# Optimization experiments

Hardware: AMD Instinct MI355X
Metric: run time of the kernel (lower is better)

The kernel has to match this reference:

```python
import jax, jax.numpy as jnp
import numpy as np

BRANCH = [True, False] * 10  # branchLs: joints that also emit a tracking frame
TRACK_IDX = np.where(np.array(BRANCH))[0]


def rpy2r(rpy):
    # rpy (..., 3) -> rotation (..., 3, 3), R = Rz(yaw) @ Ry(pitch) @ Rx(roll)
    r, p, y = rpy[..., 0], rpy[..., 1], rpy[..., 2]
    cr, sr = jnp.cos(r), jnp.sin(r)
    cp, sp = jnp.cos(p), jnp.sin(p)
    cy, sy = jnp.cos(y), jnp.sin(y)
    return jnp.stack([
        jnp.stack([cy * cp, cy * sp * sr - sy * cr, cy * sp * cr + sy * sr], -1),
        jnp.stack([sy * cp, sy * sp * sr + cy * cr, sy * sp * cr - cy * sr], -1),
        jnp.stack([-sp, cp * sr, cp * cr], -1)], -2)


def pr2t(p, R):
    # p (...,3), R (...,3,3) -> homogeneous transform (...,4,4)
    top = jnp.concatenate([R, p[..., None]], axis=-1)
    bot = jnp.broadcast_to(jnp.array([0., 0., 0., 1.], R.dtype), top.shape[:-2] + (1, 4))
    return jnp.concatenate([top, bot], axis=-2)


def rodrigues(axis, q):
    # axis (J,3) (normalized inside), q (B,J) angles -> (B,J,3,3)
    a = axis / (jnp.linalg.norm(axis, axis=-1, keepdims=True) + 1e-12)
    ax, ay, az = a[..., 0], a[..., 1], a[..., 2]
    z = jnp.zeros_like(ax)
    K = jnp.stack([jnp.stack([z, -az, ay], -1),
                   jnp.stack([az, z, -ax], -1),
                   jnp.stack([-ay, ax, z], -1)], -2)  # (J,3,3)
    K2 = K @ K
    s = jnp.sin(q)[..., None, None]  # (B,J,1,1)
    c = jnp.cos(q)[..., None, None]
    return jnp.eye(3, dtype=q.dtype) + s * K + (1. - c) * K2


def _forward(rev_q, pri_q, rev_p_off, rev_rpy_off, pri_p_off, pri_rpy_off,
             rev_axis, pri_axis, p_track, rpy_track):
    B, J = rev_q.shape
    dt = rev_q.dtype
    rev_T_off = pr2t(rev_p_off, rpy2r(rev_rpy_off))    # (J,4,4)
    pri_T_off = pr2t(pri_p_off, rpy2r(pri_rpy_off))    # (J,4,4)
    T_track = pr2t(p_track, rpy2r(rpy_track))          # (J,4,4)
    rev_T = pr2t(jnp.zeros((B, J, 3), dt), rodrigues(rev_axis, rev_q))  # (B,J,4,4)
    eye3 = jnp.broadcast_to(jnp.eye(3, dtype=dt), (B, J, 3, 3))
    pri_T = pr2t(pri_q[..., None] * pri_axis[None], eye3)               # (B,J,4,4)
    # fold constant offsets into per-joint steps, joint axis leading for scan
    rev_step = jnp.einsum('jab,njbc->jnac', rev_T_off, rev_T)  # (J,B,4,4)
    pri_step = jnp.einsum('jab,njbc->jnac', pri_T_off, pri_T)  # (J,B,4,4)

    def step(out, xs):
        rs, ps, tt = xs
        out1 = out @ rs          # after revolute joint
        out2 = out1 @ ps         # after prismatic joint
        return out2, (out1, out2, out2 @ tt)

    init = jnp.broadcast_to(jnp.eye(4, dtype=dt), (B, 4, 4))
    _, (rev_all, pri_all, trk_all) = jax.lax.scan(step, init, (rev_step, pri_step, T_track))
    RevSE3 = jnp.transpose(rev_all, (1, 0, 2, 3))                  # (B,J,4,4)
    PriSE3 = jnp.transpose(pri_all, (1, 0, 2, 3))                  # (B,J,4,4)
    TrackingSE3 = jnp.transpose(trk_all[TRACK_IDX], (1, 0, 2, 3))  # (B,n_track,4,4)
    return TrackingSE3, RevSE3, PriSE3


def setup_inputs() -> dict:
    key = jax.random.key(0)
    ks = jax.random.split(key, 10)
    B, J = 32768, 20
    u = lambda k, s: jax.random.uniform(k, s, jnp.float32, -1., 1.)
    return {
        'rev_q_value': jax.random.normal(ks[0], (B, J), jnp.float32),
        'pri_q_value': jax.random.normal(ks[1], (B, J), jnp.float32),
        'rev_p_offset': u(ks[2], (J, 3)), 'rev_rpy_offset': u(ks[3], (J, 3)),
        'pri_p_offset': u(ks[4], (J, 3)), 'pri_rpy_offset': u(ks[5], (J, 3)),
        'rev_axis': u(ks[6], (J, 3)), 'pri_axis': u(ks[7], (J, 3)),
        'p_track': u(ks[8], (J, 3)), 'rpy_track': u(ks[9], (J, 3)),
    }


def reference(rev_q_value, pri_q_value, rev_p_offset, rev_rpy_offset,
              pri_p_offset, pri_rpy_offset, rev_axis, pri_axis, p_track, rpy_track):
    return _forward(rev_q_value, pri_q_value, rev_p_offset, rev_rpy_offset,
                    pri_p_offset, pri_rpy_offset, rev_axis, pri_axis, p_track, rpy_track)
```

## Files before the change

kernel.cpp:

```cpp
#include <hip/hip_runtime.h>
#include <math.h>


constexpr int NJ = 20;

__device__ __forceinline__ void rpy2r_dev(float r, float p, float y, float R[9]) {
    float sr, cr, sp, cp, sy, cy;
    __sincosf(r, &sr, &cr);
    __sincosf(p, &sp, &cp);
    __sincosf(y, &sy, &cy);
    R[0] = cy * cp; R[1] = cy * sp * sr - sy * cr; R[2] = cy * sp * cr + sy * sr;
    R[3] = sy * cp; R[4] = sy * sp * sr + cy * cr; R[5] = sy * sp * cr - cy * sr;
    R[6] = -sp;     R[7] = cp * sr;                R[8] = cp * cr;
}

__device__ __forceinline__ void mat33_mul(const float A[9], const float B[9], float C[9]) {
#pragma unroll
    for (int i = 0; i < 3; ++i) {
        C[3 * i + 0] = A[3 * i + 0] * B[0] + A[3 * i + 1] * B[3] + A[3 * i + 2] * B[6];
        C[3 * i + 1] = A[3 * i + 0] * B[1] + A[3 * i + 1] * B[4] + A[3 * i + 2] * B[7];
        C[3 * i + 2] = A[3 * i + 0] * B[2] + A[3 * i + 1] * B[5] + A[3 * i + 2] * B[8];
    }
}

__global__ __launch_bounds__(64) void fk_kernel(
    const float* __restrict__ rev_q,      const float* __restrict__ pri_q,
    const float* __restrict__ rev_p_off,  const float* __restrict__ rev_rpy_off,
    const float* __restrict__ pri_p_off,  const float* __restrict__ pri_rpy_off,
    const float* __restrict__ rev_axis,   const float* __restrict__ pri_axis,
    const float* __restrict__ p_track,    const float* __restrict__ rpy_track,
    float* __restrict__ out, int B)
{
    __shared__ float4 cst[NJ][11];
    const int t = threadIdx.x;

    if (t < NJ) {
        const int j = t;
        float Ro[9], Rp[9], Rt[9];
        rpy2r_dev(rev_rpy_off[3 * j], rev_rpy_off[3 * j + 1], rev_rpy_off[3 * j + 2], Ro);
        rpy2r_dev(pri_rpy_off[3 * j], pri_rpy_off[3 * j + 1], pri_rpy_off[3 * j + 2], Rp);
        rpy2r_dev(rpy_track[3 * j],   rpy_track[3 * j + 1],   rpy_track[3 * j + 2],   Rt);
        cst[j][0] = make_float4(Ro[0], Ro[1], Ro[2], rev_p_off[3 * j + 0]);
        cst[j][1] = make_float4(Ro[3], Ro[4], Ro[5], rev_p_off[3 * j + 1]);
        cst[j][2] = make_float4(Ro[6], Ro[7], Ro[8], rev_p_off[3 * j + 2]);
        cst[j][3] = make_float4(Rp[0], Rp[1], Rp[2], pri_p_off[3 * j + 0]);
        cst[j][4] = make_float4(Rp[3], Rp[4], Rp[5], pri_p_off[3 * j + 1]);
        cst[j][5] = make_float4(Rp[6], Rp[7], Rp[8], pri_p_off[3 * j + 2]);
        cst[j][6] = make_float4(Rt[0], Rt[1], Rt[2], p_track[3 * j + 0]);
        cst[j][7] = make_float4(Rt[3], Rt[4], Rt[5], p_track[3 * j + 1]);
        cst[j][8] = make_float4(Rt[6], Rt[7], Rt[8], p_track[3 * j + 2]);
        const float ax = rev_axis[3 * j], ay = rev_axis[3 * j + 1], az = rev_axis[3 * j + 2];
        const float inv = 1.0f / (sqrtf(ax * ax + ay * ay + az * az) + 1e-12f);
        cst[j][9] = make_float4(ax * inv, ay * inv, az * inv, 0.0f);
        const float px = pri_axis[3 * j], py = pri_axis[3 * j + 1], pz = pri_axis[3 * j + 2];
        cst[j][10] = make_float4(Rp[0] * px + Rp[1] * py + Rp[2] * pz,
                                 Rp[3] * px + Rp[4] * py + Rp[5] * pz,
                                 Rp[6] * px + Rp[7] * py + Rp[8] * pz, 0.0f);
    }
    __syncthreads();

    const int b = blockIdx.x * 64 + t;
    if (b >= B) return;

    float rq[NJ], pq[NJ];
    {
        const float4* r4 = reinterpret_cast<const float4*>(rev_q + (size_t)b * NJ);
        const float4* p4 = reinterpret_cast<const float4*>(pri_q + (size_t)b * NJ);
#pragma unroll
        for (int i = 0; i < NJ / 4; ++i) {
            float4 a = r4[i];
            rq[4 * i + 0] = a.x; rq[4 * i + 1] = a.y; rq[4 * i + 2] = a.z; rq[4 * i + 3] = a.w;
            float4 c = p4[i];
            pq[4 * i + 0] = c.x; pq[4 * i + 1] = c.y; pq[4 * i + 2] = c.z; pq[4 * i + 3] = c.w;
        }
    }

    float TR[9] = {1, 0, 0, 0, 1, 0, 0, 0, 1};
    float Tp[3] = {0, 0, 0};

    float4* out4 = reinterpret_cast<float4*>(out);
    const size_t trkBase = (size_t)b * 40;
    const size_t revBase = (size_t)B * 40 + (size_t)b * 80;
    const size_t priBase = (size_t)B * 120 + (size_t)b * 80;

#pragma unroll
    for (int j = 0; j < NJ; ++j) {
        float s, c;
        __sincosf(rq[j], &s, &c);
        const float4 a4 = cst[j][9];
        const float ax = a4.x, ay = a4.y, az = a4.z;
        const float omc = 1.0f - c;
        float Rr[9];
        Rr[0] = c + omc * ax * ax;      Rr[1] = omc * ax * ay - s * az; Rr[2] = omc * ax * az + s * ay;
        Rr[3] = omc * ax * ay + s * az; Rr[4] = c + omc * ay * ay;      Rr[5] = omc * ay * az - s * ax;
        Rr[6] = omc * ax * az - s * ay; Rr[7] = omc * ay * az + s * ax; Rr[8] = c + omc * az * az;

        const float4 cr0 = cst[j][0], cr1 = cst[j][1], cr2 = cst[j][2];
        const float Roff[9] = {cr0.x, cr0.y, cr0.z, cr1.x, cr1.y, cr1.z, cr2.x, cr2.y, cr2.z};
        float Ra[9], R1[9], p1[3];
        mat33_mul(TR, Roff, Ra);
        mat33_mul(Ra, Rr, R1);
#pragma unroll
        for (int i = 0; i < 3; ++i)
            p1[i] = fmaf(TR[3 * i + 0], cr0.w,
                    fmaf(TR[3 * i + 1], cr1.w,
                    fmaf(TR[3 * i + 2], cr2.w, Tp[i])));

        out4[revBase + 4 * j + 0] = make_float4(R1[0], R1[1], R1[2], p1[0]);
        out4[revBase + 4 * j + 1] = make_float4(R1[3], R1[4], R1[5], p1[1]);
        out4[revBase + 4 * j + 2] = make_float4(R1[6], R1[7], R1[8], p1[2]);
        out4[revBase + 4 * j + 3] = make_float4(0.f, 0.f, 0.f, 1.f);

        const float4 cp0 = cst[j][3], cp1 = cst[j][4], cp2 = cst[j][5];
        const float4 w4 = cst[j][10];
        const float qp = pq[j];
        const float pstep[3] = {fmaf(qp, w4.x, cp0.w), fmaf(qp, w4.y, cp1.w), fmaf(qp, w4.z, cp2.w)};
        const float Rpoff[9] = {cp0.x, cp0.y, cp0.z, cp1.x, cp1.y, cp1.z, cp2.x, cp2.y, cp2.z};
        float R2[9], p2[3];
        mat33_mul(R1, Rpoff, R2);
#pragma unroll
        for (int i = 0; i < 3; ++i)
            p2[i] = fmaf(R1[3 * i + 0], pstep[0],
                    fmaf(R1[3 * i + 1], pstep[1],
                    fmaf(R1[3 * i + 2], pstep[2], p1[i])));

        out4[priBase + 4 * j + 0] = make_float4(R2[0], R2[1], R2[2], p2[0]);
        out4[priBase + 4 * j + 1] = make_float4(R2[3], R2[4], R2[5], p2[1]);
        out4[priBase + 4 * j + 2] = make_float4(R2[6], R2[7], R2[8], p2[2]);
        out4[priBase + 4 * j + 3] = make_float4(0.f, 0.f, 0.f, 1.f);

        if ((j & 1) == 0) {
            const float4 ct0 = cst[j][6], ct1 = cst[j][7], ct2 = cst[j][8];
            const float Rtrk[9] = {ct0.x, ct0.y, ct0.z, ct1.x, ct1.y, ct1.z, ct2.x, ct2.y, ct2.z};
            float R3[9], p3[3];
            mat33_mul(R2, Rtrk, R3);
#pragma unroll
            for (int i = 0; i < 3; ++i)
                p3[i] = fmaf(R2[3 * i + 0], ct0.w,
                        fmaf(R2[3 * i + 1], ct1.w,
                        fmaf(R2[3 * i + 2], ct2.w, p2[i])));
            const size_t tb = trkBase + 4 * (size_t)(j >> 1);
            out4[tb + 0] = make_float4(R3[0], R3[1], R3[2], p3[0]);
            out4[tb + 1] = make_float4(R3[3], R3[4], R3[5], p3[1]);
            out4[tb + 2] = make_float4(R3[6], R3[7], R3[8], p3[2]);
            out4[tb + 3] = make_float4(0.f, 0.f, 0.f, 1.f);
        }

#pragma unroll
        for (int i = 0; i < 9; ++i) TR[i] = R2[i];
#pragma unroll
        for (int i = 0; i < 3; ++i) Tp[i] = p2[i];
    }
}

extern "C" void kernel_launch(void* const* d_in, const int* in_sizes, int n_in,
                              void* d_out, int out_size, void* d_ws, size_t ws_size,
                              hipStream_t stream) {
    (void)n_in; (void)out_size; (void)d_ws; (void)ws_size;
    const float* rev_q       = (const float*)d_in[0];
    const float* pri_q       = (const float*)d_in[1];
    const float* rev_p_off   = (const float*)d_in[2];
    const float* rev_rpy_off = (const float*)d_in[3];
    const float* pri_p_off   = (const float*)d_in[4];
    const float* pri_rpy_off = (const float*)d_in[5];
    const float* rev_axis    = (const float*)d_in[6];
    const float* pri_axis    = (const float*)d_in[7];
    const float* p_track     = (const float*)d_in[8];
    const float* rpy_track   = (const float*)d_in[9];

    const int B = in_sizes[0] / NJ;
    const int blocks = (B + 63) / 64;
    fk_kernel<<<dim3(blocks), dim3(64), 0, stream>>>(
        rev_q, pri_q, rev_p_off, rev_rpy_off, pri_p_off, pri_rpy_off,
        rev_axis, pri_axis, p_track, rpy_track, (float*)d_out, B);
}
```

Measured before the change: 169.3 us.

## Split FK into prefix-transform pass and parallel per-joint output pass

The kernel now runs in two phases. First, 64 threads compute the serial chain of prefix transforms per batch element and store them in LDS. Then all 256 threads process the (batch, joint) pairs independently, recomputing each joint's rev/pri/track transforms from the stored prefix and writing outputs. This exposes more parallelism for the store-heavy output phase and makes writes across threads more interleaved. The cost is duplicated per-joint math, about 60KB of shared memory per block (which limits occupancy), and 3/4 of the threads sitting idle during the serial phase.

```diff
diff --git a/kernel.cpp b/kernel.cpp
--- a/kernel.cpp
+++ b/kernel.cpp
@@ -3,6 +3,8 @@
 
 
 constexpr int NJ = 20;
+constexpr int GB = 64;
+constexpr int PREF_STRIDE = 61;
 
 __device__ __forceinline__ void rpy2r_dev(float r, float p, float y, float R[9]) {
     float sr, cr, sp, cp, sy, cy;
@@ -23,7 +25,7 @@
     }
 }
 
-__global__ __launch_bounds__(64) void fk_kernel(
+__global__ __launch_bounds__(256) void fk_kernel(
     const float* __restrict__ rev_q,      const float* __restrict__ pri_q,
     const float* __restrict__ rev_p_off,  const float* __restrict__ rev_rpy_off,
     const float* __restrict__ pri_p_off,  const float* __restrict__ pri_rpy_off,
@@ -32,6 +34,10 @@
     float* __restrict__ out, int B)
 {
     __shared__ float4 cst[NJ][11];
+    __shared__ float4 pre4[GB * PREF_STRIDE];
+    __shared__ float  sRq[GB * NJ];
+    __shared__ float  sPq[GB * NJ];
+
     const int t = threadIdx.x;
 
     if (t < NJ) {
@@ -59,37 +65,87 @@
     }
     __syncthreads();
 
-    const int b = blockIdx.x * 64 + t;
-    if (b >= B) return;
-
-    float rq[NJ], pq[NJ];
-    {
-        const float4* r4 = reinterpret_cast<const float4*>(rev_q + (size_t)b * NJ);
-        const float4* p4 = reinterpret_cast<const float4*>(pri_q + (size_t)b * NJ);
-#pragma unroll
-        for (int i = 0; i < NJ / 4; ++i) {
-            float4 a = r4[i];
-            rq[4 * i + 0] = a.x; rq[4 * i + 1] = a.y; rq[4 * i + 2] = a.z; rq[4 * i + 3] = a.w;
-            float4 c = p4[i];
-            pq[4 * i + 0] = c.x; pq[4 * i + 1] = c.y; pq[4 * i + 2] = c.z; pq[4 * i + 3] = c.w;
+    const int blockBase = blockIdx.x * GB;
+
+    if (t < GB) {
+        const int b = blockBase + t;
+        if (b < B) {
+            float rq[NJ], pq[NJ];
+            const float4* r4 = reinterpret_cast<const float4*>(rev_q + (size_t)b * NJ);
+            const float4* p4 = reinterpret_cast<const float4*>(pri_q + (size_t)b * NJ);
+            float4* sR4 = reinterpret_cast<float4*>(&sRq[t * NJ]);
+            float4* sP4 = reinterpret_cast<float4*>(&sPq[t * NJ]);
+#pragma unroll
+            for (int i = 0; i < NJ / 4; ++i) {
+                float4 a = r4[i]; sR4[i] = a;
+                rq[4 * i] = a.x; rq[4 * i + 1] = a.y; rq[4 * i + 2] = a.z; rq[4 * i + 3] = a.w;
+                float4 c = p4[i]; sP4[i] = c;
+                pq[4 * i] = c.x; pq[4 * i + 1] = c.y; pq[4 * i + 2] = c.z; pq[4 * i + 3] = c.w;
+            }
+
+            float TR[9] = {1, 0, 0, 0, 1, 0, 0, 0, 1};
+            float Tp[3] = {0, 0, 0};
+#pragma unroll
+            for (int j = 0; j < NJ; ++j) {
+                float4* pr = &pre4[t * PREF_STRIDE + j * 3];
+                pr[0] = make_float4(TR[0], TR[1], TR[2], Tp[0]);
+                pr[1] = make_float4(TR[3], TR[4], TR[5], Tp[1]);
+                pr[2] = make_float4(TR[6], TR[7], TR[8], Tp[2]);
+
+                float s, c;
+                __sincosf(rq[j], &s, &c);
+                const float4 a4 = cst[j][9];
+                const float ax = a4.x, ay = a4.y, az = a4.z, omc = 1.0f - c;
+                float Rr[9];
+                Rr[0] = c + omc * ax * ax;      Rr[1] = omc * ax * ay - s * az; Rr[2] = omc * ax * az + s * ay;
+                Rr[3] = omc * ax * ay + s * az; Rr[4] = c + omc * ay * ay;      Rr[5] = omc * ay * az - s * ax;
+                Rr[6] = omc * ax * az - s * ay; Rr[7] = omc * ay * az + s * ax; Rr[8] = c + omc * az * az;
+
+                const float4 cr0 = cst[j][0], cr1 = cst[j][1], cr2 = cst[j][2];
+                const float Roff[9] = {cr0.x, cr0.y, cr0.z, cr1.x, cr1.y, cr1.z, cr2.x, cr2.y, cr2.z};
+                float Ra[9], R1[9], p1[3];
+                mat33_mul(TR, Roff, Ra);
+                mat33_mul(Ra, Rr, R1);
+#pragma unroll
+                for (int i = 0; i < 3; ++i)
+                    p1[i] = fmaf(TR[3 * i], cr0.w, fmaf(TR[3 * i + 1], cr1.w, fmaf(TR[3 * i + 2], cr2.w, Tp[i])));
+
+                const float4 cp0 = cst[j][3], cp1 = cst[j][4], cp2 = cst[j][5];
+                const float4 w4 = cst[j][10];
+                const float qp = pq[j];
+                const float pstep[3] = {fmaf(qp, w4.x, cp0.w), fmaf(qp, w4.y, cp1.w), fmaf(qp, w4.z, cp2.w)};
+                const float Rpoff[9] = {cp0.x, cp0.y, cp0.z, cp1.x, cp1.y, cp1.z, cp2.x, cp2.y, cp2.z};
+                float R2[9];
+                mat33_mul(R1, Rpoff, R2);
+#pragma unroll
+                for (int i = 0; i < 3; ++i)
+                    Tp[i] = fmaf(R1[3 * i], pstep[0], fmaf(R1[3 * i + 1], pstep[1], fmaf(R1[3 * i + 2], pstep[2], p1[i])));
+#pragma unroll
+                for (int i = 0; i < 9; ++i) TR[i] = R2[i];
+            }
         }
     }
-
-    float TR[9] = {1, 0, 0, 0, 1, 0, 0, 0, 1};
-    float Tp[3] = {0, 0, 0};
+    __syncthreads();
 
     float4* out4 = reinterpret_cast<float4*>(out);
-    const size_t trkBase = (size_t)b * 40;
-    const size_t revBase = (size_t)B * 40 + (size_t)b * 80;
-    const size_t priBase = (size_t)B * 120 + (size_t)b * 80;
-
-#pragma unroll
-    for (int j = 0; j < NJ; ++j) {
+    const int npairs = GB * NJ;
+#pragma unroll
+    for (int it = 0; it < npairs / 256; ++it) {
+        const int p = it * 256 + t;
+        const int bl = (p * 3277) >> 16;
+        const int j = p - bl * 20;
+        const int b = blockBase + bl;
+        if (b >= B) continue;
+
+        const float4* pr = &pre4[bl * PREF_STRIDE + j * 3];
+        const float4 t0 = pr[0], t1 = pr[1], t2 = pr[2];
+        const float TbR[9] = {t0.x, t0.y, t0.z, t1.x, t1.y, t1.z, t2.x, t2.y, t2.z};
+        const float Tbp[3] = {t0.w, t1.w, t2.w};
+
         float s, c;
-        __sincosf(rq[j], &s, &c);
+        __sincosf(sRq[bl * NJ + j], &s, &c);
         const float4 a4 = cst[j][9];
-        const float ax = a4.x, ay = a4.y, az = a4.z;
-        const float omc = 1.0f - c;
+        const float ax = a4.x, ay = a4.y, az = a4.z, omc = 1.0f - c;
         float Rr[9];
         Rr[0] = c + omc * ax * ax;      Rr[1] = omc * ax * ay - s * az; Rr[2] = omc * ax * az + s * ay;
         Rr[3] = omc * ax * ay + s * az; Rr[4] = c + omc * ay * ay;      Rr[5] = omc * ay * az - s * ax;
@@ -98,36 +154,34 @@
         const float4 cr0 = cst[j][0], cr1 = cst[j][1], cr2 = cst[j][2];
         const float Roff[9] = {cr0.x, cr0.y, cr0.z, cr1.x, cr1.y, cr1.z, cr2.x, cr2.y, cr2.z};
         float Ra[9], R1[9], p1[3];
-        mat33_mul(TR, Roff, Ra);
+        mat33_mul(TbR, Roff, Ra);
         mat33_mul(Ra, Rr, R1);
 #pragma unroll
         for (int i = 0; i < 3; ++i)
-            p1[i] = fmaf(TR[3 * i + 0], cr0.w,
-                    fmaf(TR[3 * i + 1], cr1.w,
-                    fmaf(TR[3 * i + 2], cr2.w, Tp[i])));
-
-        out4[revBase + 4 * j + 0] = make_float4(R1[0], R1[1], R1[2], p1[0]);
-        out4[revBase + 4 * j + 1] = make_float4(R1[3], R1[4], R1[5], p1[1]);
-        out4[revBase + 4 * j + 2] = make_float4(R1[6], R1[7], R1[8], p1[2]);
-        out4[revBase + 4 * j + 3] = make_float4(0.f, 0.f, 0.f, 1.f);
+            p1[i] = fmaf(TbR[3 * i], cr0.w, fmaf(TbR[3 * i + 1], cr1.w, fmaf(TbR[3 * i + 2], cr2.w, Tbp[i])));
+
+        const size_t revBase = (size_t)B * 40 + (size_t)b * 80 + (size_t)j * 4;
+        out4[revBase + 0] = make_float4(R1[0], R1[1], R1[2], p1[0]);
+        out4[revBase + 1] = make_float4(R1[3], R1[4], R1[5], p1[1]);
+        out4[revBase + 2] = make_float4(R1[6], R1[7], R1[8], p1[2]);
+        out4[revBase + 3] = make_float4(0.f, 0.f, 0.f, 1.f);
 
         const float4 cp0 = cst[j][3], cp1 = cst[j][4], cp2 = cst[j][5];
         const float4 w4 = cst[j][10];
-        const float qp = pq[j];
+        const float qp = sPq[bl * NJ + j];
         const float pstep[3] = {fmaf(qp, w4.x, cp0.w), fmaf(qp, w4.y, cp1.w), fmaf(qp, w4.z, cp2.w)};
         const float Rpoff[9] = {cp0.x, cp0.y, cp0.z, cp1.x, cp1.y, cp1.z, cp2.x, cp2.y, cp2.z};
         float R2[9], p2[3];
         mat33_mul(R1, Rpoff, R2);
 #pragma unroll
         for (int i = 0; i < 3; ++i)
-            p2[i] = fmaf(R1[3 * i + 0], pstep[0],
-                    fmaf(R1[3 * i + 1], pstep[1],
-                    fmaf(R1[3 * i + 2], pstep[2], p1[i])));
-
-        out4[priBase + 4 * j + 0] = make_float4(R2[0], R2[1], R2[2], p2[0]);
-        out4[priBase + 4 * j + 1] = make_float4(R2[3], R2[4], R2[5], p2[1]);
-        out4[priBase + 4 * j + 2] = make_float4(R2[6], R2[7], R2[8], p2[2]);
-        out4[priBase + 4 * j + 3] = make_float4(0.f, 0.f, 0.f, 1.f);
+            p2[i] = fmaf(R1[3 * i], pstep[0], fmaf(R1[3 * i + 1], pstep[1], fmaf(R1[3 * i + 2], pstep[2], p1[i])));
+
+        const size_t priBase = (size_t)B * 120 + (size_t)b * 80 + (size_t)j * 4;
+        out4[priBase + 0] = make_float4(R2[0], R2[1], R2[2], p2[0]);
+        out4[priBase + 1] = make_float4(R2[3], R2[4], R2[5], p2[1]);
+        out4[priBase + 2] = make_float4(R2[6], R2[7], R2[8], p2[2]);
+        out4[priBase + 3] = make_float4(0.f, 0.f, 0.f, 1.f);
 
         if ((j & 1) == 0) {
             const float4 ct0 = cst[j][6], ct1 = cst[j][7], ct2 = cst[j][8];
@@ -136,20 +190,13 @@
             mat33_mul(R2, Rtrk, R3);
 #pragma unroll
             for (int i = 0; i < 3; ++i)
-                p3[i] = fmaf(R2[3 * i + 0], ct0.w,
-                        fmaf(R2[3 * i + 1], ct1.w,
-                        fmaf(R2[3 * i + 2], ct2.w, p2[i])));
-            const size_t tb = trkBase + 4 * (size_t)(j >> 1);
+                p3[i] = fmaf(R2[3 * i], ct0.w, fmaf(R2[3 * i + 1], ct1.w, fmaf(R2[3 * i + 2], ct2.w, p2[i])));
+            const size_t tb = (size_t)b * 40 + (size_t)(j >> 1) * 4;
             out4[tb + 0] = make_float4(R3[0], R3[1], R3[2], p3[0]);
             out4[tb + 1] = make_float4(R3[3], R3[4], R3[5], p3[1]);
             out4[tb + 2] = make_float4(R3[6], R3[7], R3[8], p3[2]);
             out4[tb + 3] = make_float4(0.f, 0.f, 0.f, 1.f);
         }
-
-#pragma unroll
-        for (int i = 0; i < 9; ++i) TR[i] = R2[i];
-#pragma unroll
-        for (int i = 0; i < 3; ++i) Tp[i] = p2[i];
     }
 }
 
@@ -169,8 +216,8 @@
     const float* rpy_track   = (const float*)d_in[9];
 
     const int B = in_sizes[0] / NJ;
-    const int blocks = (B + 63) / 64;
-    fk_kernel<<<dim3(blocks), dim3(64), 0, stream>>>(
+    const int blocks = (B + GB - 1) / GB;
+    fk_kernel<<<dim3(blocks), dim3(256), 0, stream>>>(
         rev_q, pri_q, rev_p_off, rev_rpy_off, pri_p_off, pri_rpy_off,
         rev_axis, pri_axis, p_track, rpy_track, (float*)d_out, B);
 }
```

Result: faster. 152.0 us (-10.2%).

## Parallelize joint chain with wave-level prefix scan over affine transforms

Applied to the files above, without the earlier changes.

Replaces the per-thread sequential 20-joint forward-kinematics loop with one lane per (batch, joint). Each lane builds its local step transform, and an inclusive prefix scan over 3x4 affine compositions runs via __shfl_up across 32-lane segments. This spreads the serial dependency chain across lanes and makes adjacent lanes write adjacent joint matrices, which coalesces stores. In exchange it does more total arithmetic (log-step composes and many shuffles) and leaves 12 of every 32 lanes idle.

```diff
diff --git a/kernel.cpp b/kernel.cpp
--- a/kernel.cpp
+++ b/kernel.cpp
@@ -3,6 +3,9 @@
 
 
 constexpr int NJ = 20;
+constexpr int BPB = 8;
+
+struct Aff { float R[9]; float p[3]; };
 
 __device__ __forceinline__ void rpy2r_dev(float r, float p, float y, float R[9]) {
     float sr, cr, sp, cp, sy, cy;
@@ -23,7 +26,27 @@
     }
 }
 
-__global__ __launch_bounds__(64) void fk_kernel(
+__device__ __forceinline__ Aff compose(const Aff& A, const Aff& B) {
+    Aff C;
+    mat33_mul(A.R, B.R, C.R);
+#pragma unroll
+    for (int i = 0; i < 3; ++i)
+        C.p[i] = fmaf(A.R[3 * i + 0], B.p[0],
+                 fmaf(A.R[3 * i + 1], B.p[1],
+                 fmaf(A.R[3 * i + 2], B.p[2], A.p[i])));
+    return C;
+}
+
+__device__ __forceinline__ Aff shfl_up_aff(const Aff& V, int d) {
+    Aff N;
+#pragma unroll
+    for (int k = 0; k < 9; ++k) N.R[k] = __shfl_up(V.R[k], d, 32);
+#pragma unroll
+    for (int k = 0; k < 3; ++k) N.p[k] = __shfl_up(V.p[k], d, 32);
+    return N;
+}
+
+__global__ __launch_bounds__(256) void fk_scan_kernel(
     const float* __restrict__ rev_q,      const float* __restrict__ pri_q,
     const float* __restrict__ rev_p_off,  const float* __restrict__ rev_rpy_off,
     const float* __restrict__ pri_p_off,  const float* __restrict__ pri_rpy_off,
@@ -59,97 +82,84 @@
     }
     __syncthreads();
 
-    const int b = blockIdx.x * 64 + t;
-    if (b >= B) return;
+    const int j = t & 31;
+    const int b = blockIdx.x * BPB + (t >> 5);
+    if (j >= NJ || b >= B) return;
 
-    float rq[NJ], pq[NJ];
-    {
-        const float4* r4 = reinterpret_cast<const float4*>(rev_q + (size_t)b * NJ);
-        const float4* p4 = reinterpret_cast<const float4*>(pri_q + (size_t)b * NJ);
+    const float rq = rev_q[(size_t)b * NJ + j];
+    const float pq = pri_q[(size_t)b * NJ + j];
+
+    float s, c;
+    __sincosf(rq, &s, &c);
+    const float4 a4 = cst[j][9];
+    const float ax = a4.x, ay = a4.y, az = a4.z, omc = 1.0f - c;
+    float Rr[9];
+    Rr[0] = c + omc * ax * ax;      Rr[1] = omc * ax * ay - s * az; Rr[2] = omc * ax * az + s * ay;
+    Rr[3] = omc * ax * ay + s * az; Rr[4] = c + omc * ay * ay;      Rr[5] = omc * ay * az - s * ax;
+    Rr[6] = omc * ax * az - s * ay; Rr[7] = omc * ay * az + s * ax; Rr[8] = c + omc * az * az;
+
+    const float4 cr0 = cst[j][0], cr1 = cst[j][1], cr2 = cst[j][2];
+    const float Roff[9] = {cr0.x, cr0.y, cr0.z, cr1.x, cr1.y, cr1.z, cr2.x, cr2.y, cr2.z};
+    Aff revstep;
+    mat33_mul(Roff, Rr, revstep.R);
+    revstep.p[0] = cr0.w; revstep.p[1] = cr1.w; revstep.p[2] = cr2.w;
+
+    const float4 cp0 = cst[j][3], cp1 = cst[j][4], cp2 = cst[j][5];
+    const float4 w4 = cst[j][10];
+    const float Rpoff[9] = {cp0.x, cp0.y, cp0.z, cp1.x, cp1.y, cp1.z, cp2.x, cp2.y, cp2.z};
+    const float pp[3] = {fmaf(pq, w4.x, cp0.w), fmaf(pq, w4.y, cp1.w), fmaf(pq, w4.z, cp2.w)};
+
+    Aff V;
+    mat33_mul(revstep.R, Rpoff, V.R);
 #pragma unroll
-        for (int i = 0; i < NJ / 4; ++i) {
-            float4 a = r4[i];
-            rq[4 * i + 0] = a.x; rq[4 * i + 1] = a.y; rq[4 * i + 2] = a.z; rq[4 * i + 3] = a.w;
-            float4 c = p4[i];
-            pq[4 * i + 0] = c.x; pq[4 * i + 1] = c.y; pq[4 * i + 2] = c.z; pq[4 * i + 3] = c.w;
-        }
+    for (int i = 0; i < 3; ++i)
+        V.p[i] = fmaf(revstep.R[3 * i + 0], pp[0],
+                 fmaf(revstep.R[3 * i + 1], pp[1],
+                 fmaf(revstep.R[3 * i + 2], pp[2], revstep.p[i])));
+
+#pragma unroll
+    for (int d = 1; d < 32; d <<= 1) {
+        Aff N = shfl_up_aff(V, d);
+        if (j >= d) V = compose(N, V);
     }
 
-    float TR[9] = {1, 0, 0, 0, 1, 0, 0, 0, 1};
-    float Tp[3] = {0, 0, 0};
+    Aff P = shfl_up_aff(V, 1);
+    if (j == 0) {
+        P.R[0] = 1.f; P.R[1] = 0.f; P.R[2] = 0.f;
+        P.R[3] = 0.f; P.R[4] = 1.f; P.R[5] = 0.f;
+        P.R[6] = 0.f; P.R[7] = 0.f; P.R[8] = 1.f;
+        P.p[0] = 0.f; P.p[1] = 0.f; P.p[2] = 0.f;
+    }
+    const Aff Rev = compose(P, revstep);
 
     float4* out4 = reinterpret_cast<float4*>(out);
-    const size_t trkBase = (size_t)b * 40;
-    const size_t revBase = (size_t)B * 40 + (size_t)b * 80;
-    const size_t priBase = (size_t)B * 120 + (size_t)b * 80;
+    const float4 bot = make_float4(0.f, 0.f, 0.f, 1.f);
 
-#pragma unroll
-    for (int j = 0; j < NJ; ++j) {
-        float s, c;
-        __sincosf(rq[j], &s, &c);
-        const float4 a4 = cst[j][9];
-        const float ax = a4.x, ay = a4.y, az = a4.z;
-        const float omc = 1.0f - c;
-        float Rr[9];
-        Rr[0] = c + omc * ax * ax;      Rr[1] = omc * ax * ay - s * az; Rr[2] = omc * ax * az + s * ay;
-        Rr[3] = omc * ax * ay + s * az; Rr[4] = c + omc * ay * ay;      Rr[5] = omc * ay * az - s * ax;
-        Rr[6] = omc * ax * az - s * ay; Rr[7] = omc * ay * az + s * ax; Rr[8] = c + omc * az * az;
+    const size_t revBase = (size_t)B * 40 + (size_t)b * 80 + (size_t)j * 4;
+    out4[revBase + 0] = make_float4(Rev.R[0], Rev.R[1], Rev.R[2], Rev.p[0]);
+    out4[revBase + 1] = make_float4(Rev.R[3], Rev.R[4], Rev.R[5], Rev.p[1]);
+    out4[revBase + 2] = make_float4(Rev.R[6], Rev.R[7], Rev.R[8], Rev.p[2]);
+    out4[revBase + 3] = bot;
 
-        const float4 cr0 = cst[j][0], cr1 = cst[j][1], cr2 = cst[j][2];
-        const float Roff[9] = {cr0.x, cr0.y, cr0.z, cr1.x, cr1.y, cr1.z, cr2.x, cr2.y, cr2.z};
-        float Ra[9], R1[9], p1[3];
-        mat33_mul(TR, Roff, Ra);
-        mat33_mul(Ra, Rr, R1);
-#pragma unroll
-        for (int i = 0; i < 3; ++i)
-            p1[i] = fmaf(TR[3 * i + 0], cr0.w,
-                    fmaf(TR[3 * i + 1], cr1.w,
-                    fmaf(TR[3 * i + 2], cr2.w, Tp[i])));
+    const size_t priBase = (size_t)B * 120 + (size_t)b * 80 + (size_t)j * 4;
+    out4[priBase + 0] = make_float4(V.R[0], V.R[1], V.R[2], V.p[0]);
+    out4[priBase + 1] = make_float4(V.R[3], V.R[4], V.R[5], V.p[1]);
+    out4[priBase + 2] = make_float4(V.R[6], V.R[7], V.R[8], V.p[2]);
+    out4[priBase + 3] = bot;
 
-        out4[revBase + 4 * j + 0] = make_float4(R1[0], R1[1], R1[2], p1[0]);
-        out4[revBase + 4 * j + 1] = make_float4(R1[3], R1[4], R1[5], p1[1]);
-        out4[revBase + 4 * j + 2] = make_float4(R1[6], R1[7], R1[8], p1[2]);
-        out4[revBase + 4 * j + 3] = make_float4(0.f, 0.f, 0.f, 1.f);
-
-        const float4 cp0 = cst[j][3], cp1 = cst[j][4], cp2 = cst[j][5];
-        const float4 w4 = cst[j][10];
-        const float qp = pq[j];
-        const float pstep[3] = {fmaf(qp, w4.x, cp0.w), fmaf(qp, w4.y, cp1.w), fmaf(qp, w4.z, cp2.w)};
-        const float Rpoff[9] = {cp0.x, cp0.y, cp0.z, cp1.x, cp1.y, cp1.z, cp2.x, cp2.y, cp2.z};
-        float R2[9], p2[3];
-        mat33_mul(R1, Rpoff, R2);
-#pragma unroll
-        for (int i = 0; i < 3; ++i)
-            p2[i] = fmaf(R1[3 * i + 0], pstep[0],
-                    fmaf(R1[3 * i + 1], pstep[1],
-                    fmaf(R1[3 * i + 2], pstep[2], p1[i])));
-
-        out4[priBase + 4 * j + 0] = make_float4(R2[0], R2[1], R2[2], p2[0]);
-        out4[priBase + 4 * j + 1] = make_float4(R2[3], R2[4], R2[5], p2[1]);
-        out4[priBase + 4 * j + 2] = make_float4(R2[6], R2[7], R2[8], p2[2]);
-        out4[priBase + 4 * j + 3] = make_float4(0.f, 0.f, 0.f, 1.f);
-
-        if ((j & 1) == 0) {
-            const float4 ct0 = cst[j][6], ct1 = cst[j][7], ct2 = cst[j][8];
-            const float Rtrk[9] = {ct0.x, ct0.y, ct0.z, ct1.x, ct1.y, ct1.z, ct2.x, ct2.y, ct2.z};
-            float R3[9], p3[3];
-            mat33_mul(R2, Rtrk, R3);
-#pragma unroll
-            for (int i = 0; i < 3; ++i)
-                p3[i] = fmaf(R2[3 * i + 0], ct0.w,
-                        fmaf(R2[3 * i + 1], ct1.w,
-                        fmaf(R2[3 * i + 2], ct2.w, p2[i])));
-            const size_t tb = trkBase + 4 * (size_t)(j >> 1);
-            out4[tb + 0] = make_float4(R3[0], R3[1], R3[2], p3[0]);
-            out4[tb + 1] = make_float4(R3[3], R3[4], R3[5], p3[1]);
-            out4[tb + 2] = make_float4(R3[6], R3[7], R3[8], p3[2]);
-            out4[tb + 3] = make_float4(0.f, 0.f, 0.f, 1.f);
-        }
-
-#pragma unroll
-        for (int i = 0; i < 9; ++i) TR[i] = R2[i];
-#pragma unroll
-        for (int i = 0; i < 3; ++i) Tp[i] = p2[i];
+    if ((j & 1) == 0) {
+        const float4 ct0 = cst[j][6], ct1 = cst[j][7], ct2 = cst[j][8];
+        Aff T;
+        T.R[0] = ct0.x; T.R[1] = ct0.y; T.R[2] = ct0.z;
+        T.R[3] = ct1.x; T.R[4] = ct1.y; T.R[5] = ct1.z;
+        T.R[6] = ct2.x; T.R[7] = ct2.y; T.R[8] = ct2.z;
+        T.p[0] = ct0.w; T.p[1] = ct1.w; T.p[2] = ct2.w;
+        const Aff Trk = compose(V, T);
+        const size_t tb = (size_t)b * 40 + (size_t)(j >> 1) * 4;
+        out4[tb + 0] = make_float4(Trk.R[0], Trk.R[1], Trk.R[2], Trk.p[0]);
+        out4[tb + 1] = make_float4(Trk.R[3], Trk.R[4], Trk.R[5], Trk.p[1]);
+        out4[tb + 2] = make_float4(Trk.R[6], Trk.R[7], Trk.R[8], Trk.p[2]);
+        out4[tb + 3] = bot;
     }
 }
 
@@ -169,8 +179,8 @@
     const float* rpy_track   = (const float*)d_in[9];
 
     const int B = in_sizes[0] / NJ;
-    const int blocks = (B + 63) / 64;
-    fk_kernel<<<dim3(blocks), dim3(64), 0, stream>>>(
+    const int blocks = (B + BPB - 1) / BPB;
+    fk_scan_kernel<<<dim3(blocks), dim3(256), 0, stream>>>(
         rev_q, pri_q, rev_p_off, rev_rpy_off, pri_p_off, pri_rpy_off,
         rev_axis, pri_axis, p_track, rpy_track, (float*)d_out, B);
 }
```

New measurement: 149.9 us. 11.5% less time.
